# Kernel optimization log

Hardware: AMD Instinct MI355X
Metric: run time of the kernel (lower is better)

## Reference

```python
import jax, jax.numpy as jnp
import numpy as np

B, N, CIN, COUT = 4, 4096, 64, 64

def setup_inputs() -> dict:
    key = jax.random.key(0)
    k1, k2, k3, k4, k5 = jax.random.split(key, 5)
    X = jax.random.normal(k1, (B, N, CIN), dtype=jnp.float32)
    A = jax.random.uniform(k2, (N, N), dtype=jnp.float32)
    weight1 = jax.random.normal(k3, (CIN, COUT), dtype=jnp.float32) * 0.05
    weight2 = jax.random.normal(k4, (1 * COUT, COUT), dtype=jnp.float32) * 0.05
    alpha = jax.random.normal(k5, (2 * COUT, 1), dtype=jnp.float32) * 0.05
    return {"X": X, "A": A, "weight1": weight1, "weight2": weight2, "alpha": alpha}

def reference(X, A, weight1, weight2, alpha):
    n = A.shape[0]
    c = weight1.shape[1]
    b = X.shape[0]
    # add self loops on the adjacency diagonal
    idx = jnp.arange(n)
    adj = A.at[idx, idx].set(1.0)
    # node transform: [B,N,C]
    out = jnp.matmul(X, weight1)
    # edge feature (P=1): [N,N,1], row-normalized over j (axis=1)
    E = adj[:, :, None]
    E_wave = E / E.sum(axis=1, keepdims=True)
    # attention scores via rank-1 decomposition of alpha
    att_l = jnp.matmul(out, alpha[:c])   # [B,N,1]
    att_r = jnp.matmul(out, alpha[c:])   # [B,N,1]
    scores = jax.nn.leaky_relu(att_l @ jnp.swapaxes(att_r, 1, 2))  # [B,N,N]
    # exp + edge-feature weighting: [P,B,N,N]
    att = jnp.einsum('bij,ijp->pbij', jnp.exp(scores), E_wave)
    # manual softmax-style normalization over neighbors j
    att = att / att.sum(axis=-1, keepdims=True)
    # aggregate: [B,N,P,C] -> [B,N,P*C]
    agg = jnp.einsum('pbij,bjc->bipc', att, out).reshape(b, n, -1)
    return jnp.matmul(agg, weight2)
```

## Files before the change

### kernel.cpp

```cpp
#include <hip/hip_runtime.h>
#include <hip/hip_bf16.h>

typedef __attribute__((ext_vector_type(8))) short short8;
typedef __attribute__((ext_vector_type(4))) float floatx4;

#define NN 4096

static __device__ __forceinline__ unsigned f2bf_rne(float x) {
    union { float f; unsigned u; } v; v.f = x;
    unsigned r = v.u + 0x7fffu + ((v.u >> 16) & 1u);
    return r >> 16;
}
static __device__ __forceinline__ float bf2f(unsigned hi) {
    union { unsigned u; float f; } v; v.u = hi << 16; return v.f;
}

__global__ void wc_kernel(const float* __restrict__ W1,
                          const float* __restrict__ W2,
                          const float* __restrict__ alpha,
                          unsigned short* __restrict__ Wfb,
                          float* __restrict__ w1a) {
    __shared__ float red[4][64];
    const int k = blockIdx.x;
    const int t = threadIdx.x;
    const int c = t & 63, mq = t >> 6;
    float p = 0.f;
    #pragma unroll
    for (int mm = 0; mm < 16; ++mm) {
        int mrow = mq * 16 + mm;
        p += W1[k * 64 + mrow] * W2[mrow * 64 + c];
    }
    red[mq][c] = p;
    __syncthreads();
    if (t < 64) {
        float wcv = (red[0][t] + red[1][t]) + (red[2][t] + red[3][t]);
        Wfb[t * 64 + k] = (unsigned short)f2bf_rne(wcv);
        float v = W1[k * 64 + t];
        float pl = v * alpha[t], pr = v * alpha[64 + t];
        #pragma unroll
        for (int off = 32; off > 0; off >>= 1) {
            pl += __shfl_xor(pl, off, 64);
            pr += __shfl_xor(pr, off, 64);
        }
        if (t == 0) { w1a[k] = pl; w1a[64 + k] = pr; }
    }
}

__global__ __launch_bounds__(256, 4)
void prep_kernel(const float* __restrict__ X,
                 const unsigned short* __restrict__ Wfb,
                 const float* __restrict__ w1a,
                 unsigned short* __restrict__ Gt,
                 float* __restrict__ lv,
                 float* __restrict__ rv) {
    __shared__ float w1s[128];
    __shared__ float Gs[64][68];
    const int t = threadIdx.x;
    const int row0 = blockIdx.x * 64;
    const int b = row0 >> 12, n0 = row0 & (NN - 1);
    const int w = t >> 6, lane = t & 63;
    const int m = lane & 15, q = lane >> 4;
    if (t < 128) w1s[t] = w1a[t];

    const int row = row0 + w * 16 + m;
    const float* xp = X + (size_t)row * 64;
    float4 x0 = *(const float4*)(xp + q * 8);
    float4 x1 = *(const float4*)(xp + q * 8 + 4);
    float4 x2 = *(const float4*)(xp + 32 + q * 8);
    float4 x3 = *(const float4*)(xp + 32 + q * 8 + 4);
    const float xs[16] = {x0.x,x0.y,x0.z,x0.w, x1.x,x1.y,x1.z,x1.w,
                          x2.x,x2.y,x2.z,x2.w, x3.x,x3.y,x3.z,x3.w};
    __syncthreads();

    float pl = 0.f, pr = 0.f;
    #pragma unroll
    for (int ks = 0; ks < 2; ++ks)
        #pragma unroll
        for (int j = 0; j < 8; ++j) {
            int k = ks * 32 + q * 8 + j;
            float xv = xs[ks * 8 + j];
            pl += xv * w1s[k];
            pr += xv * w1s[64 + k];
        }
    pl += __shfl_xor(pl, 16, 64); pl += __shfl_xor(pl, 32, 64);
    pr += __shfl_xor(pr, 16, 64); pr += __shfl_xor(pr, 32, 64);
    if (q == 0) { lv[row] = pl; rv[row] = pr; }

    short8 ah[2], al[2];
    #pragma unroll
    for (int ks = 0; ks < 2; ++ks)
        #pragma unroll
        for (int j = 0; j < 8; ++j) {
            float f = xs[ks * 8 + j];
            unsigned hb = f2bf_rne(f);
            float res = f - bf2f(hb);
            ah[ks][j] = (short)hb;
            al[ks][j] = (short)f2bf_rne(res);
        }

    floatx4 acc[4] = {{0,0,0,0},{0,0,0,0},{0,0,0,0},{0,0,0,0}};
    #pragma unroll
    for (int ks = 0; ks < 2; ++ks)
        #pragma unroll
        for (int nt = 0; nt < 4; ++nt) {
            short8 bf = *(const short8*)(Wfb + (nt * 16 + m) * 64 + ks * 32 + q * 8);
            acc[nt] = __builtin_amdgcn_mfma_f32_16x16x32_bf16(ah[ks], bf, acc[nt], 0, 0, 0);
            acc[nt] = __builtin_amdgcn_mfma_f32_16x16x32_bf16(al[ks], bf, acc[nt], 0, 0, 0);
        }

    #pragma unroll
    for (int nt = 0; nt < 4; ++nt)
        #pragma unroll
        for (int rg = 0; rg < 4; ++rg)
            Gs[nt * 16 + m][w * 16 + q * 4 + rg] = acc[nt][rg];
    __syncthreads();
    unsigned* Gu = (unsigned*)Gt;
    #pragma unroll
    for (int it2 = 0; it2 < 8; ++it2) {
        int c2 = (t >> 5) + it2 * 8;
        int np = t & 31;
        unsigned lo = f2bf_rne(Gs[c2][2 * np]);
        unsigned hi = f2bf_rne(Gs[c2][2 * np + 1]);
        Gu[(((((size_t)(b * 64 + c2)) << 12) + n0) >> 1) + np] = lo | (hi << 16);
    }
}

__global__ __launch_bounds__(256, 4)
void attn_kernel(const float* __restrict__ A,
                 const unsigned short* __restrict__ Gt,
                 const float* __restrict__ lv,
                 const float* __restrict__ rv,
                 float* __restrict__ num,
                 float* __restrict__ den) {
    __shared__ float rs[1024];
    __shared__ float lis[64];
    __shared__ __align__(16) unsigned short Es[64 * 40];
    __shared__ __align__(16) unsigned short Gs[64 * 40];
    const int bx = blockIdx.x;
    const int i0 = (bx & 63) * 64;
    const int b  = (bx >> 6) & 3;
    const int jbase = (bx >> 8) * 1024;
    const int t = threadIdx.x;
    const int w = t >> 6, lane = t & 63;
    const int m = lane & 15, q = lane >> 4;
    const int irow = t >> 2;
    const int jseg = t & 3;

    *(float4*)&rs[t * 4] = *(const float4*)(rv + b * NN + jbase + t * 4);
    if (t < 64) lis[t] = lv[b * NN + i0 + t] * 1.44269504f;

    const float* aRow = A + (size_t)(i0 + irow) * NN + jbase + jseg * 8;
    const unsigned short* gRow = Gt + (((size_t)(b * 64 + irow)) << 12) + jbase + jseg * 8;
    const int ii = i0 + irow;

    __syncthreads();
    const float li = lis[irow];

    floatx4 acc0 = {0,0,0,0}, acc1 = {0,0,0,0}, acc2 = {0,0,0,0}, acc3 = {0,0,0,0};
    float denp = 0.f;

    float4 pa0 = *(const float4*)(aRow);
    float4 pa1 = *(const float4*)(aRow + 4);
    uint4  pg  = *(const uint4*)(gRow);

    for (int jj = 0; jj < 1024; jj += 32) {
        float4 a0 = pa0, a1 = pa1;
        uint4 g = pg;
        const int jn = (jj + 32 < 1024) ? jj + 32 : jj;
        pa0 = *(const float4*)(aRow + jn);
        pa1 = *(const float4*)(aRow + jn + 4);
        pg  = *(const uint4*)(gRow + jn);

        const float av[8] = {a0.x, a0.y, a0.z, a0.w, a1.x, a1.y, a1.z, a1.w};
        const float* rp = &rs[jj + jseg * 8];
        const int jglob = jbase + jj + jseg * 8;
        unsigned up[8];
        #pragma unroll
        for (int e = 0; e < 8; ++e) {
            float aa = (jglob + e == ii) ? 1.0f : av[e];
            float s2 = li * rp[e];
            s2 = fmaxf(s2, 0.01f * s2);
            float ev = exp2f(s2) * aa;
            denp += ev;
            up[e] = __float_as_uint(ev) + 0x8000u;
        }
        uint4 epk;
        epk.x = __builtin_amdgcn_perm(up[1], up[0], 0x07060302u);
        epk.y = __builtin_amdgcn_perm(up[3], up[2], 0x07060302u);
        epk.z = __builtin_amdgcn_perm(up[5], up[4], 0x07060302u);
        epk.w = __builtin_amdgcn_perm(up[7], up[6], 0x07060302u);

        __syncthreads();
        *(uint4*)&Es[irow * 40 + jseg * 8] = epk;
        *(uint4*)&Gs[irow * 40 + jseg * 8] = g;
        __syncthreads();

        short8 afr = *(const short8*)&Es[(w * 16 + m) * 40 + q * 8];
        short8 b0  = *(const short8*)&Gs[(m)      * 40 + q * 8];
        short8 b1  = *(const short8*)&Gs[(16 + m) * 40 + q * 8];
        short8 b2  = *(const short8*)&Gs[(32 + m) * 40 + q * 8];
        short8 b3  = *(const short8*)&Gs[(48 + m) * 40 + q * 8];
        acc0 = __builtin_amdgcn_mfma_f32_16x16x32_bf16(afr, b0, acc0, 0, 0, 0);
        acc1 = __builtin_amdgcn_mfma_f32_16x16x32_bf16(afr, b1, acc1, 0, 0, 0);
        acc2 = __builtin_amdgcn_mfma_f32_16x16x32_bf16(afr, b2, acc2, 0, 0, 0);
        acc3 = __builtin_amdgcn_mfma_f32_16x16x32_bf16(afr, b3, acc3, 0, 0, 0);
    }

    denp += __shfl_xor(denp, 1, 64);
    denp += __shfl_xor(denp, 2, 64);
    if ((lane & 3) == 0) atomicAdd(&den[b * NN + ii], denp);

    #pragma unroll
    for (int nt = 0; nt < 4; ++nt) {
        floatx4 acc = nt == 0 ? acc0 : nt == 1 ? acc1 : nt == 2 ? acc2 : acc3;
        #pragma unroll
        for (int rg = 0; rg < 4; ++rg) {
            int ir = i0 + w * 16 + q * 4 + rg;
            int cc = nt * 16 + m;
            atomicAdd(&num[((size_t)(b * NN + ir) << 6) + cc], acc[rg]);
        }
    }
}

__global__ void out_kernel(const float* __restrict__ num,
                           const float* __restrict__ den,
                           float* __restrict__ out) {
    int i4 = blockIdx.x * 256 + threadIdx.x;
    float4 v = ((const float4*)num)[i4];
    float r = 1.0f / den[i4 >> 4];
    float4 o; o.x = v.x * r; o.y = v.y * r; o.z = v.z * r; o.w = v.w * r;
    ((float4*)out)[i4] = o;
}

extern "C" void kernel_launch(void* const* d_in, const int* in_sizes, int n_in,
                              void* d_out, int out_size, void* d_ws, size_t ws_size,
                              hipStream_t stream) {
    const float* X     = (const float*)d_in[0];
    const float* A     = (const float*)d_in[1];
    const float* W1    = (const float*)d_in[2];
    const float* W2    = (const float*)d_in[3];
    const float* alpha = (const float*)d_in[4];
    float* out = (float*)d_out;

    char* ws = (char*)d_ws;
    unsigned short* Gt  = (unsigned short*)(ws);
    float* lvp = (float*)(ws + 2097152);
    float* rvp = (float*)(ws + 2097152 + 65536);
    float* num = (float*)(ws + 2228224);
    float* den = (float*)(ws + 6422528);
    unsigned short* Wfb = (unsigned short*)(ws + 6488064);
    float* w1a = (float*)(ws + 6496256);

    hipMemsetAsync(num, 0, 4194304 + 65536, stream);
    wc_kernel<<<64, 256, 0, stream>>>(W1, W2, alpha, Wfb, w1a);
    prep_kernel<<<256, 256, 0, stream>>>(X, Wfb, w1a, Gt, lvp, rvp);
    attn_kernel<<<1024, 256, 0, stream>>>(A, Gt, lvp, rvp, num, den);
    out_kernel<<<1024, 256, 0, stream>>>(num, den, out);
}
```

Measured before the change: 150.7 us.

## Double-buffer attention tiles, split j range finer, fuse memset and denominator via MFMA

Double-buffers the Es/Gs shared tiles, which removes one barrier per iteration, and prefetches two steps ahead. The j range is halved per block so the grid doubles to 2048 blocks, and launch bounds rise to 6 waves for more occupancy. The denominator is now computed by an extra MFMA against a ones vector, using the bf16-rounded weights. The diagonal check runs only in blocks whose j range contains the diagonal, and the num/den memset is folded into wc_kernel. In exchange the kernel issues more atomics per output and adds some register pressure.

After: 272.6 us. 1.81x slower.

```diff
diff --git a/kernel.cpp b/kernel.cpp
--- a/kernel.cpp
+++ b/kernel.cpp
@@ -19,11 +19,17 @@
                           const float* __restrict__ W2,
                           const float* __restrict__ alpha,
                           unsigned short* __restrict__ Wfb,
-                          float* __restrict__ w1a) {
+                          float* __restrict__ w1a,
+                          float* __restrict__ numden) {
     __shared__ float red[4][64];
     const int k = blockIdx.x;
     const int t = threadIdx.x;
     const int c = t & 63, mq = t >> 6;
+
+    float4 z = {0.f, 0.f, 0.f, 0.f};
+    for (int idx = blockIdx.x * 256 + t; idx < 266240; idx += 64 * 256)
+        ((float4*)numden)[idx] = z;
+
     float p = 0.f;
     #pragma unroll
     for (int mm = 0; mm < 16; ++mm) {
@@ -125,90 +131,105 @@
     }
 }
 
-__global__ __launch_bounds__(256, 4)
+__global__ __launch_bounds__(256, 6)
 void attn_kernel(const float* __restrict__ A,
                  const unsigned short* __restrict__ Gt,
                  const float* __restrict__ lv,
                  const float* __restrict__ rv,
                  float* __restrict__ num,
                  float* __restrict__ den) {
-    __shared__ float rs[1024];
+    __shared__ float rs[512];
     __shared__ float lis[64];
-    __shared__ __align__(16) unsigned short Es[64 * 40];
-    __shared__ __align__(16) unsigned short Gs[64 * 40];
+    __shared__ __align__(16) unsigned short Es[2][64 * 40];
+    __shared__ __align__(16) unsigned short Gs[2][64 * 40];
     const int bx = blockIdx.x;
     const int i0 = (bx & 63) * 64;
     const int b  = (bx >> 6) & 3;
-    const int jbase = (bx >> 8) * 1024;
+    const int js = bx >> 8;
+    const int jbase = js * 512;
     const int t = threadIdx.x;
     const int w = t >> 6, lane = t & 63;
     const int m = lane & 15, q = lane >> 4;
-    const int irow = t >> 2;
-    const int jseg = t & 3;
-
-    *(float4*)&rs[t * 4] = *(const float4*)(rv + b * NN + jbase + t * 4);
+    const int irow = t >> 2, jseg = t & 3;
+    const bool hasdiag = ((i0 >> 9) == js);
+
+    *(float2*)&rs[t * 2] = *(const float2*)(rv + b * NN + jbase + t * 2);
     if (t < 64) lis[t] = lv[b * NN + i0 + t] * 1.44269504f;
 
     const float* aRow = A + (size_t)(i0 + irow) * NN + jbase + jseg * 8;
     const unsigned short* gRow = Gt + (((size_t)(b * 64 + irow)) << 12) + jbase + jseg * 8;
     const int ii = i0 + irow;
-
     __syncthreads();
     const float li = lis[irow];
 
-    floatx4 acc0 = {0,0,0,0}, acc1 = {0,0,0,0}, acc2 = {0,0,0,0}, acc3 = {0,0,0,0};
-    float denp = 0.f;
-
-    float4 pa0 = *(const float4*)(aRow);
-    float4 pa1 = *(const float4*)(aRow + 4);
-    uint4  pg  = *(const uint4*)(gRow);
-
-    for (int jj = 0; jj < 1024; jj += 32) {
-        float4 a0 = pa0, a1 = pa1;
-        uint4 g = pg;
-        const int jn = (jj + 32 < 1024) ? jj + 32 : jj;
-        pa0 = *(const float4*)(aRow + jn);
-        pa1 = *(const float4*)(aRow + jn + 4);
-        pg  = *(const uint4*)(gRow + jn);
-
-        const float av[8] = {a0.x, a0.y, a0.z, a0.w, a1.x, a1.y, a1.z, a1.w};
+    floatx4 acc0 = {0,0,0,0}, acc1 = {0,0,0,0}, acc2 = {0,0,0,0},
+            acc3 = {0,0,0,0}, accd = {0,0,0,0};
+    short8 ones;
+    #pragma unroll
+    for (int e = 0; e < 8; ++e) ones[e] = (short)0x3F80;
+
+    float4 Pa0[2], Pa1[2]; uint4 Pg[2];
+    Pa0[0] = *(const float4*)(aRow);
+    Pa1[0] = *(const float4*)(aRow + 4);
+    Pg[0]  = *(const uint4*)(gRow);
+    Pa0[1] = *(const float4*)(aRow + 32);
+    Pa1[1] = *(const float4*)(aRow + 36);
+    Pg[1]  = *(const uint4*)(gRow + 32);
+
+    for (int jj = 0; jj < 512; jj += 32) {
+        const int s = (jj >> 5) & 1;
+        float4 a0 = Pa0[s], a1 = Pa1[s];
+        uint4 g = Pg[s];
+        const int jn = (jj + 64 < 512) ? jj + 64 : jj;
+        Pa0[s] = *(const float4*)(aRow + jn);
+        Pa1[s] = *(const float4*)(aRow + jn + 4);
+        Pg[s]  = *(const uint4*)(gRow + jn);
+
+        float aa[8] = {a0.x, a0.y, a0.z, a0.w, a1.x, a1.y, a1.z, a1.w};
+        if (hasdiag) {
+            const int jglob = jbase + jj + jseg * 8;
+            #pragma unroll
+            for (int e = 0; e < 8; ++e)
+                if (jglob + e == ii) aa[e] = 1.0f;
+        }
         const float* rp = &rs[jj + jseg * 8];
-        const int jglob = jbase + jj + jseg * 8;
-        unsigned up[8];
-        #pragma unroll
-        for (int e = 0; e < 8; ++e) {
-            float aa = (jglob + e == ii) ? 1.0f : av[e];
-            float s2 = li * rp[e];
-            s2 = fmaxf(s2, 0.01f * s2);
-            float ev = exp2f(s2) * aa;
-            denp += ev;
-            up[e] = __float_as_uint(ev) + 0x8000u;
-        }
         uint4 epk;
-        epk.x = __builtin_amdgcn_perm(up[1], up[0], 0x07060302u);
-        epk.y = __builtin_amdgcn_perm(up[3], up[2], 0x07060302u);
-        epk.z = __builtin_amdgcn_perm(up[5], up[4], 0x07060302u);
-        epk.w = __builtin_amdgcn_perm(up[7], up[6], 0x07060302u);
-
+        unsigned ew[4];
+        #pragma unroll
+        for (int e2 = 0; e2 < 4; ++e2) {
+            float sl = li * rp[2 * e2];
+            float sh = li * rp[2 * e2 + 1];
+            sl = fmaxf(sl, 0.01f * sl);
+            sh = fmaxf(sh, 0.01f * sh);
+            float el = exp2f(sl) * aa[2 * e2];
+            float eh = exp2f(sh) * aa[2 * e2 + 1];
+            unsigned ul = __float_as_uint(el) + 0x8000u;
+            unsigned uh = __float_as_uint(eh) + 0x8000u;
+            ew[e2] = __builtin_amdgcn_perm(uh, ul, 0x07060302u);
+        }
+        epk.x = ew[0]; epk.y = ew[1]; epk.z = ew[2]; epk.w = ew[3];
+
+        *(uint4*)&Es[s][irow * 40 + jseg * 8] = epk;
+        *(uint4*)&Gs[s][irow * 40 + jseg * 8] = g;
         __syncthreads();
-        *(uint4*)&Es[irow * 40 + jseg * 8] = epk;
-        *(uint4*)&Gs[irow * 40 + jseg * 8] = g;
-        __syncthreads();
-
-        short8 afr = *(const short8*)&Es[(w * 16 + m) * 40 + q * 8];
-        short8 b0  = *(const short8*)&Gs[(m)      * 40 + q * 8];
-        short8 b1  = *(const short8*)&Gs[(16 + m) * 40 + q * 8];
-        short8 b2  = *(const short8*)&Gs[(32 + m) * 40 + q * 8];
-        short8 b3  = *(const short8*)&Gs[(48 + m) * 40 + q * 8];
+
+        short8 afr = *(const short8*)&Es[s][(w * 16 + m) * 40 + q * 8];
+        short8 b0  = *(const short8*)&Gs[s][(m)      * 40 + q * 8];
+        short8 b1  = *(const short8*)&Gs[s][(16 + m) * 40 + q * 8];
+        short8 b2  = *(const short8*)&Gs[s][(32 + m) * 40 + q * 8];
+        short8 b3  = *(const short8*)&Gs[s][(48 + m) * 40 + q * 8];
         acc0 = __builtin_amdgcn_mfma_f32_16x16x32_bf16(afr, b0, acc0, 0, 0, 0);
         acc1 = __builtin_amdgcn_mfma_f32_16x16x32_bf16(afr, b1, acc1, 0, 0, 0);
         acc2 = __builtin_amdgcn_mfma_f32_16x16x32_bf16(afr, b2, acc2, 0, 0, 0);
         acc3 = __builtin_amdgcn_mfma_f32_16x16x32_bf16(afr, b3, acc3, 0, 0, 0);
-    }
-
-    denp += __shfl_xor(denp, 1, 64);
-    denp += __shfl_xor(denp, 2, 64);
-    if ((lane & 3) == 0) atomicAdd(&den[b * NN + ii], denp);
+        accd = __builtin_amdgcn_mfma_f32_16x16x32_bf16(afr, ones, accd, 0, 0, 0);
+    }
+
+    if (m == 0) {
+        #pragma unroll
+        for (int rg = 0; rg < 4; ++rg)
+            atomicAdd(&den[b * NN + i0 + w * 16 + q * 4 + rg], accd[rg]);
+    }
 
     #pragma unroll
     for (int nt = 0; nt < 4; ++nt) {
@@ -251,9 +272,8 @@
     unsigned short* Wfb = (unsigned short*)(ws + 6488064);
     float* w1a = (float*)(ws + 6496256);
 
-    hipMemsetAsync(num, 0, 4194304 + 65536, stream);
-    wc_kernel<<<64, 256, 0, stream>>>(W1, W2, alpha, Wfb, w1a);
+    wc_kernel<<<64, 256, 0, stream>>>(W1, W2, alpha, Wfb, w1a, num);
     prep_kernel<<<256, 256, 0, stream>>>(X, Wfb, w1a, Gt, lvp, rvp);
-    attn_kernel<<<1024, 256, 0, stream>>>(A, Gt, lvp, rvp, num, den);
+    attn_kernel<<<2048, 256, 0, stream>>>(A, Gt, lvp, rvp, num, den);
     out_kernel<<<1024, 256, 0, stream>>>(num, den, out);
 }
```
